# Kernel optimization log

Measured on AMD Instinct MI355X. Metric: run time of the kernel, lower is better.

Reference implementation:

```python
import jax, jax.numpy as jnp
import numpy as np

DIM = 1024
HEADS = 16
HEAD_DIM = DIM // HEADS

def setup_inputs() -> dict:
    key = jax.random.key(0)
    ks = jax.random.split(key, 6)
    s = 0.02
    return {
        "x": jax.random.normal(ks[0], (2, 2048, DIM), dtype=jnp.float32),
        "w_qkv": jax.random.normal(ks[1], (DIM, 3 * DIM), dtype=jnp.float32) * s,
        "w_proj": jax.random.normal(ks[2], (DIM, DIM), dtype=jnp.float32) * s,
        "b_proj": jnp.zeros((DIM,), dtype=jnp.float32),
        "ln_gamma": jnp.ones((DIM,), dtype=jnp.float32),
        "ln_beta": jnp.zeros((DIM,), dtype=jnp.float32),
    }

def layer_norm(x, gamma, beta, eps=1e-5):
    mu = jnp.mean(x, axis=-1, keepdims=True)
    var = jnp.var(x, axis=-1, keepdims=True)
    return (x - mu) * jax.lax.rsqrt(var + eps) * gamma + beta

def reference(x, w_qkv, w_proj, b_proj, ln_gamma, ln_beta):
    B, N, C = x.shape
    residual = x
    h = layer_norm(x, ln_gamma, ln_beta)
    qkv = h @ w_qkv  # [B,N,3C]
    qkv = qkv.reshape(B, N, 3, HEADS, HEAD_DIM)
    q = jnp.transpose(qkv[:, :, 0], (0, 2, 1, 3))  # [B,H,N,D]
    k = jnp.transpose(qkv[:, :, 1], (0, 2, 1, 3))
    v = jnp.transpose(qkv[:, :, 2], (0, 2, 1, 3))
    scale = 1.0 / jnp.sqrt(jnp.float32(HEAD_DIM))
    attn = jnp.einsum('bhqd,bhkd->bhqk', q, k) * scale
    attn = jax.nn.softmax(attn, axis=-1)
    out = jnp.einsum('bhqk,bhkd->bhqd', attn, v)  # [B,H,N,D]
    out = jnp.transpose(out, (0, 2, 1, 3)).reshape(B, N, C)
    out = out @ w_proj + b_proj
    return out + residual
```

## Files before the change

### kernel.cpp

```cpp
#include <hip/hip_runtime.h>

#define DIM   1024
#define HEADS 16
#define HDIM  64
#define BATCH 2
#define SEQ   2048
#define TOK   (BATCH*SEQ)
#define MEG   1048576

typedef __bf16 bf16x8 __attribute__((ext_vector_type(8)));
typedef float  f32x4  __attribute__((ext_vector_type(4)));

__device__ __forceinline__ float b2f(ushort u) {
    union { unsigned int u32; float f; } x; x.u32 = ((unsigned int)u) << 16; return x.f;
}
__device__ __forceinline__ ushort f2b(float f) {
    union { float f; unsigned int u32; } x; x.f = f;
    unsigned int r = x.u32 + 0x7FFFu + ((x.u32 >> 16) & 1u);
    return (ushort)(r >> 16);
}
__device__ __forceinline__ ushort f2b_t(float f) {
    union { float f; unsigned int u32; } x; x.f = f;
    return (ushort)(x.u32 >> 16);
}
__device__ __forceinline__ void gload_lds16(const ushort* g, void* l) {
    __builtin_amdgcn_global_load_lds((const __attribute__((address_space(1))) void*)g,
                                     (__attribute__((address_space(3))) void*)l, 16, 0, 0);
}

__global__ void transpose_f2b_k(const float* __restrict__ src, ushort* __restrict__ dst,
                                int R, int Cc) {
    __shared__ ushort tile[32][33];
    int c0 = blockIdx.x * 32, r0 = blockIdx.y * 32;
    int tx = threadIdx.x, ty = threadIdx.y;
#pragma unroll
    for (int i = 0; i < 4; i++)
        tile[ty + 8 * i][tx] = f2b(src[(long)(r0 + ty + 8 * i) * Cc + c0 + tx]);
    __syncthreads();
#pragma unroll
    for (int i = 0; i < 4; i++)
        dst[(long)(c0 + ty + 8 * i) * R + r0 + tx] = tile[tx][ty + 8 * i];
}

__global__ void transpose_bf16_k(const ushort* __restrict__ src, ushort* __restrict__ dst,
                                 int R, int Cc, long sstride, long dstride) {
    __shared__ ushort tile[32][33];
    long b = blockIdx.z;
    const ushort* s = src + b * sstride;
    ushort* d = dst + b * dstride;
    int c0 = blockIdx.x * 32, r0 = blockIdx.y * 32;
    int tx = threadIdx.x, ty = threadIdx.y;
#pragma unroll
    for (int i = 0; i < 4; i++)
        tile[ty + 8 * i][tx] = s[(long)(r0 + ty + 8 * i) * Cc + c0 + tx];
    __syncthreads();
#pragma unroll
    for (int i = 0; i < 4; i++)
        d[(long)(c0 + ty + 8 * i) * R + r0 + tx] = tile[tx][ty + 8 * i];
}

__global__ __launch_bounds__(256)
void ln_k(const float* __restrict__ x, const float* __restrict__ gamma,
          const float* __restrict__ beta, ushort* __restrict__ h) {
    __shared__ float red[8];
    int row = blockIdx.x, tid = threadIdx.x;
    const float* xr = x + (long)row * DIM;
    float4 xv = *(const float4*)(xr + tid * 4);
    float s1 = xv.x + xv.y + xv.z + xv.w;
    float s2 = xv.x * xv.x + xv.y * xv.y + xv.z * xv.z + xv.w * xv.w;
#pragma unroll
    for (int off = 32; off; off >>= 1) {
        s1 += __shfl_down(s1, off);
        s2 += __shfl_down(s2, off);
    }
    int wid = tid >> 6, lane = tid & 63;
    if (lane == 0) { red[wid * 2] = s1; red[wid * 2 + 1] = s2; }
    __syncthreads();
    s1 = red[0] + red[2] + red[4] + red[6];
    s2 = red[1] + red[3] + red[5] + red[7];
    float mu  = s1 * (1.0f / DIM);
    float var = s2 * (1.0f / DIM) - mu * mu;
    float rs  = rsqrtf(var + 1e-5f);
    float4 gv = *(const float4*)(gamma + tid * 4);
    float4 bv = *(const float4*)(beta + tid * 4);
    ushort4 ov;
    ov.x = f2b((xv.x - mu) * rs * gv.x + bv.x);
    ov.y = f2b((xv.y - mu) * rs * gv.y + bv.y);
    ov.z = f2b((xv.z - mu) * rs * gv.z + bv.z);
    ov.w = f2b((xv.w - mu) * rs * gv.w + bv.w);
    *(ushort4*)(h + (long)row * DIM + tid * 4) = ov;
}

template <int EPI>
__global__ __launch_bounds__(256, 2)
void gemm128_k(const ushort* __restrict__ A, const ushort* __restrict__ Bt,
               int M, int N, int K,
               ushort* __restrict__ qp, ushort* __restrict__ kp, ushort* __restrict__ vp,
               const float* __restrict__ bias, const float* __restrict__ xres,
               float* __restrict__ outp) {
    __shared__ ushort As[128][32];
    __shared__ ushort Bs[128][32];
    int tid  = threadIdx.x;
    int wid  = tid >> 6, lane = tid & 63;
    int quad = lane >> 4, l16 = lane & 15;
    int wm = wid >> 1, wn = wid & 1;
    int rowbase = blockIdx.y * 128;
    int colbase = blockIdx.x * 128;
    int arow = lane >> 2;
    int acol = (lane & 3) * 8;

    f32x4 acc[4][4];
#pragma unroll
    for (int i = 0; i < 4; i++)
#pragma unroll
        for (int j = 0; j < 4; j++) acc[i][j] = (f32x4){0.f, 0.f, 0.f, 0.f};

    for (int k0 = 0; k0 < K; k0 += 32) {
#pragma unroll
        for (int p = 0; p < 2; p++) {
            int c = wid * 2 + p;
            int r = c * 16 + arow;
            const ushort* ga;
            if (EPI == 1) {
                int mm = rowbase + r, cc = k0 + acol;
                int bq = mm >> 11, nn = mm & 2047;
                int head = cc >> 6, d = cc & 63;
                ga = A + ((((long)bq * HEADS + head) * SEQ + nn) << 6) + d;
            } else {
                ga = A + (long)(rowbase + r) * K + k0 + acol;
            }
            gload_lds16(ga, &As[c * 16][0]);
            gload_lds16(Bt + (long)(colbase + r) * K + k0 + acol, &Bs[c * 16][0]);
        }
        __syncthreads();
        bf16x8 fa[4], fb[4];
#pragma unroll
        for (int t = 0; t < 4; t++)
            fa[t] = *(const bf16x8*)(&As[wm * 64 + t * 16 + l16][quad * 8]);
#pragma unroll
        for (int t = 0; t < 4; t++)
            fb[t] = *(const bf16x8*)(&Bs[wn * 64 + t * 16 + l16][quad * 8]);
#pragma unroll
        for (int i = 0; i < 4; i++)
#pragma unroll
            for (int j = 0; j < 4; j++)
                acc[i][j] = __builtin_amdgcn_mfma_f32_16x16x32_bf16(fa[i], fb[j], acc[i][j], 0, 0, 0);
        __syncthreads();
    }

#pragma unroll
    for (int i = 0; i < 4; i++)
#pragma unroll
        for (int j = 0; j < 4; j++) {
            int m0  = rowbase + wm * 64 + i * 16 + quad * 4;
            int col = colbase + wn * 64 + j * 16 + l16;
#pragma unroll
            for (int r = 0; r < 4; r++) {
                float v = acc[i][j][r];
                int mm = m0 + r;
                if (EPI == 0) {
                    int part = col >> 10, rem = col & 1023;
                    int head = rem >> 6, d = rem & 63;
                    int b = mm >> 11, nn = mm & 2047;
                    ushort* dst = (part == 0) ? qp : (part == 1) ? kp : vp;
                    float sv = (part == 0) ? v * 0.125f : v;
                    dst[((((long)b * HEADS + head) * SEQ + nn) << 6) + d] = f2b(sv);
                } else {
                    outp[(long)mm * N + col] = v + bias[col] + xres[(long)mm * N + col];
                }
            }
        }
}

__global__ __launch_bounds__(256, 4)
void attn_k(ushort* qio, const ushort* __restrict__ k,
            const ushort* __restrict__ vt) {
    __shared__ ushort Ks0[2][32][40];
    __shared__ ushort Ks1[2][32][40];
    __shared__ ushort Vs[2][64][40];
    __shared__ ushort plds[4][16][40];
    int bh = blockIdx.y;
    int tid = threadIdx.x, wid = tid >> 6, lane = tid & 63;
    int quad = lane >> 4, l16 = lane & 15;
    ushort* qh = qio + (long)bh * SEQ * HDIM;
    const ushort* kh = k  + (long)bh * SEQ * HDIM;
    const ushort* vh = vt + (long)bh * HDIM * SEQ;

    int krow = tid >> 3, kc8 = (tid & 7) * 8;
    int vrow = tid >> 2, vcol = (tid & 3) * 8;

    int qrow = blockIdx.x * 64 + wid * 16 + l16;
    bf16x8 qf0 = *(const bf16x8*)(qh + (long)qrow * HDIM + quad * 8);
    bf16x8 qf1 = *(const bf16x8*)(qh + (long)qrow * HDIM + 32 + quad * 8);

    f32x4 o[4];
#pragma unroll
    for (int dc = 0; dc < 4; dc++) o[dc] = (f32x4){0.f, 0.f, 0.f, 0.f};
    f32x4 lac0 = (f32x4){0.f, 0.f, 0.f, 0.f};
    f32x4 lac1 = (f32x4){0.f, 0.f, 0.f, 0.f};

    uint4 kreg = *(const uint4*)(kh + (long)krow * HDIM + kc8);
    uint4 vreg = *(const uint4*)(vh + (long)vrow * SEQ + vcol);
    {
        ushort* kdst = (kc8 < 32) ? &Ks0[0][krow][kc8] : &Ks1[0][krow][kc8 - 32];
        *(uint4*)kdst = kreg;
        *(uint4*)(&Vs[0][vrow][vcol]) = vreg;
    }

    const int NIT = SEQ / 32;
    for (int it = 0; it < NIT; ++it) {
        int buf = it & 1;
        if (it + 1 < NIT) {
            int kt = (it + 1) * 32;
            kreg = *(const uint4*)(kh + (long)(kt + krow) * HDIM + kc8);
            vreg = *(const uint4*)(vh + (long)vrow * SEQ + kt + vcol);
        }
        __syncthreads();

        bf16x8 kb00 = *(const bf16x8*)(&Ks0[buf][l16][quad * 8]);
        bf16x8 kb01 = *(const bf16x8*)(&Ks1[buf][l16][quad * 8]);
        bf16x8 kb10 = *(const bf16x8*)(&Ks0[buf][16 + l16][quad * 8]);
        bf16x8 kb11 = *(const bf16x8*)(&Ks1[buf][16 + l16][quad * 8]);
        f32x4 s0 = (f32x4){0.f, 0.f, 0.f, 0.f};
        f32x4 s1 = (f32x4){0.f, 0.f, 0.f, 0.f};
        s0 = __builtin_amdgcn_mfma_f32_16x16x32_bf16(qf0, kb00, s0, 0, 0, 0);
        s0 = __builtin_amdgcn_mfma_f32_16x16x32_bf16(qf1, kb01, s0, 0, 0, 0);
        s1 = __builtin_amdgcn_mfma_f32_16x16x32_bf16(qf0, kb10, s1, 0, 0, 0);
        s1 = __builtin_amdgcn_mfma_f32_16x16x32_bf16(qf1, kb11, s1, 0, 0, 0);

        float p0[4], p1[4];
#pragma unroll
        for (int r = 0; r < 4; r++) {
            p0[r] = __expf(s0[r]);
            p1[r] = __expf(s1[r]);
            lac0[r] += p0[r];
            lac1[r] += p1[r];
        }
#pragma unroll
        for (int r = 0; r < 4; r++) {
            plds[wid][quad * 4 + r][l16]      = f2b_t(p0[r]);
            plds[wid][quad * 4 + r][16 + l16] = f2b_t(p1[r]);
        }
        asm volatile("s_waitcnt lgkmcnt(0)" ::: "memory");
        bf16x8 pf = *(const bf16x8*)(&plds[wid][l16][quad * 8]);
#pragma unroll
        for (int dc = 0; dc < 4; dc++) {
            bf16x8 vfb = *(const bf16x8*)(&Vs[buf][dc * 16 + l16][quad * 8]);
            o[dc] = __builtin_amdgcn_mfma_f32_16x16x32_bf16(pf, vfb, o[dc], 0, 0, 0);
        }

        if (it + 1 < NIT) {
            ushort* kdst = (kc8 < 32) ? &Ks0[buf ^ 1][krow][kc8] : &Ks1[buf ^ 1][krow][kc8 - 32];
            *(uint4*)kdst = kreg;
            *(uint4*)(&Vs[buf ^ 1][vrow][vcol]) = vreg;
        }
    }

    float linv[4];
#pragma unroll
    for (int r = 0; r < 4; r++) {
        float t = lac0[r] + lac1[r];
        t += __shfl_xor(t, 1);
        t += __shfl_xor(t, 2);
        t += __shfl_xor(t, 4);
        t += __shfl_xor(t, 8);
        linv[r] = 1.0f / t;
    }

    int rowo = blockIdx.x * 64 + wid * 16 + quad * 4;
#pragma unroll
    for (int dc = 0; dc < 4; dc++)
#pragma unroll
        for (int r = 0; r < 4; r++)
            qh[(long)(rowo + r) * HDIM + dc * 16 + l16] = f2b(o[dc][r] * linv[r]);
}

extern "C" void kernel_launch(void* const* d_in, const int* in_sizes, int n_in,
                              void* d_out, int out_size, void* d_ws, size_t ws_size,
                              hipStream_t stream) {
    const float* x      = (const float*)d_in[0];
    const float* w_qkv  = (const float*)d_in[1];
    const float* w_proj = (const float*)d_in[2];
    const float* b_proj = (const float*)d_in[3];
    const float* gamma  = (const float*)d_in[4];
    const float* beta   = (const float*)d_in[5];
    float* out = (float*)d_out;

    ushort* ws   = (ushort*)d_ws;
    ushort* h_vt = ws;
    ushort* wqt  = ws + (size_t)4 * MEG;
    ushort* qb   = ws + (size_t)7 * MEG;
    ushort* kb   = ws + (size_t)11 * MEG;
    ushort* vb   = ws + (size_t)15 * MEG;

    transpose_f2b_k<<<dim3(3 * DIM / 32, DIM / 32), dim3(32, 8), 0, stream>>>(
        w_qkv, wqt, DIM, 3 * DIM);
    ln_k<<<dim3(TOK), dim3(256), 0, stream>>>(x, gamma, beta, h_vt);
    gemm128_k<0><<<dim3(3 * DIM / 128, TOK / 128), dim3(256), 0, stream>>>(
        h_vt, wqt, TOK, 3 * DIM, DIM, qb, kb, vb, nullptr, nullptr, nullptr);
    transpose_bf16_k<<<dim3(HDIM / 32, SEQ / 32, BATCH * HEADS), dim3(32, 8), 0, stream>>>(
        vb, h_vt, SEQ, HDIM, (long)SEQ * HDIM, (long)SEQ * HDIM);
    attn_k<<<dim3(SEQ / 64, BATCH * HEADS), dim3(256), 0, stream>>>(qb, kb, h_vt);
    transpose_f2b_k<<<dim3(DIM / 32, DIM / 32), dim3(32, 8), 0, stream>>>(
        w_proj, kb, DIM, DIM);
    gemm128_k<1><<<dim3(DIM / 128, TOK / 128), dim3(256), 0, stream>>>(
        qb, kb, TOK, DIM, DIM, nullptr, nullptr, nullptr, b_proj, x, out);
}
```

Baseline: 224.6 us.

## Process two query sub-tiles per wave in attention to reuse K/V tiles

Each wave in the attention kernel now handles 32 query rows (two 16-row sub-tiles) instead of 16, so every K and V fragment read from LDS feeds twice as many MFMAs. Blocks cover 128 queries and the grid is halved, which cuts global K/V traffic per query. The K tile is repacked into a flat padded panel array, and launch bounds are relaxed to allow more registers. The cost is fewer blocks (512) and higher register pressure, which can lower occupancy and latency hiding.

```diff
diff --git a/kernel.cpp b/kernel.cpp
--- a/kernel.cpp
+++ b/kernel.cpp
@@ -172,13 +172,12 @@
         }
 }
 
-__global__ __launch_bounds__(256, 4)
+__global__ __launch_bounds__(256, 1)
 void attn_k(ushort* qio, const ushort* __restrict__ k,
             const ushort* __restrict__ vt) {
-    __shared__ ushort Ks0[2][32][40];
-    __shared__ ushort Ks1[2][32][40];
+    __shared__ ushort Kp[2][2][1312];
     __shared__ ushort Vs[2][64][40];
-    __shared__ ushort plds[4][16][40];
+    __shared__ ushort plds[4][2][16][40];
     int bh = blockIdx.y;
     int tid = threadIdx.x, wid = tid >> 6, lane = tid & 63;
     int quad = lane >> 4, l16 = lane & 15;
@@ -187,25 +186,32 @@
     const ushort* vh = vt + (long)bh * HDIM * SEQ;
 
     int krow = tid >> 3, kc8 = (tid & 7) * 8;
+    int kpan = kc8 >> 5, kcp = kc8 & 31;
+    int koff = krow * 40 + kcp;
     int vrow = tid >> 2, vcol = (tid & 3) * 8;
 
-    int qrow = blockIdx.x * 64 + wid * 16 + l16;
-    bf16x8 qf0 = *(const bf16x8*)(qh + (long)qrow * HDIM + quad * 8);
-    bf16x8 qf1 = *(const bf16x8*)(qh + (long)qrow * HDIM + 32 + quad * 8);
-
-    f32x4 o[4];
-#pragma unroll
-    for (int dc = 0; dc < 4; dc++) o[dc] = (f32x4){0.f, 0.f, 0.f, 0.f};
-    f32x4 lac0 = (f32x4){0.f, 0.f, 0.f, 0.f};
-    f32x4 lac1 = (f32x4){0.f, 0.f, 0.f, 0.f};
+    int qrow0 = blockIdx.x * 128 + wid * 32;
+    bf16x8 qf[2][2];
+#pragma unroll
+    for (int s = 0; s < 2; s++) {
+        qf[s][0] = *(const bf16x8*)(qh + (long)(qrow0 + s * 16 + l16) * HDIM + quad * 8);
+        qf[s][1] = *(const bf16x8*)(qh + (long)(qrow0 + s * 16 + l16) * HDIM + 32 + quad * 8);
+    }
+
+    f32x4 o[2][4];
+    f32x4 lac[2][2];
+#pragma unroll
+    for (int s = 0; s < 2; s++) {
+#pragma unroll
+        for (int dc = 0; dc < 4; dc++) o[s][dc] = (f32x4){0.f, 0.f, 0.f, 0.f};
+        lac[s][0] = (f32x4){0.f, 0.f, 0.f, 0.f};
+        lac[s][1] = (f32x4){0.f, 0.f, 0.f, 0.f};
+    }
 
     uint4 kreg = *(const uint4*)(kh + (long)krow * HDIM + kc8);
     uint4 vreg = *(const uint4*)(vh + (long)vrow * SEQ + vcol);
-    {
-        ushort* kdst = (kc8 < 32) ? &Ks0[0][krow][kc8] : &Ks1[0][krow][kc8 - 32];
-        *(uint4*)kdst = kreg;
-        *(uint4*)(&Vs[0][vrow][vcol]) = vreg;
-    }
+    *(uint4*)(&Kp[0][kpan][koff]) = kreg;
+    *(uint4*)(&Vs[0][vrow][vcol]) = vreg;
 
     const int NIT = SEQ / 32;
     for (int it = 0; it < NIT; ++it) {
@@ -217,62 +223,74 @@
         }
         __syncthreads();
 
-        bf16x8 kb00 = *(const bf16x8*)(&Ks0[buf][l16][quad * 8]);
-        bf16x8 kb01 = *(const bf16x8*)(&Ks1[buf][l16][quad * 8]);
-        bf16x8 kb10 = *(const bf16x8*)(&Ks0[buf][16 + l16][quad * 8]);
-        bf16x8 kb11 = *(const bf16x8*)(&Ks1[buf][16 + l16][quad * 8]);
-        f32x4 s0 = (f32x4){0.f, 0.f, 0.f, 0.f};
-        f32x4 s1 = (f32x4){0.f, 0.f, 0.f, 0.f};
-        s0 = __builtin_amdgcn_mfma_f32_16x16x32_bf16(qf0, kb00, s0, 0, 0, 0);
-        s0 = __builtin_amdgcn_mfma_f32_16x16x32_bf16(qf1, kb01, s0, 0, 0, 0);
-        s1 = __builtin_amdgcn_mfma_f32_16x16x32_bf16(qf0, kb10, s1, 0, 0, 0);
-        s1 = __builtin_amdgcn_mfma_f32_16x16x32_bf16(qf1, kb11, s1, 0, 0, 0);
-
-        float p0[4], p1[4];
-#pragma unroll
-        for (int r = 0; r < 4; r++) {
-            p0[r] = __expf(s0[r]);
-            p1[r] = __expf(s1[r]);
-            lac0[r] += p0[r];
-            lac1[r] += p1[r];
-        }
-#pragma unroll
-        for (int r = 0; r < 4; r++) {
-            plds[wid][quad * 4 + r][l16]      = f2b_t(p0[r]);
-            plds[wid][quad * 4 + r][16 + l16] = f2b_t(p1[r]);
-        }
+        bf16x8 kb[2][2];
+#pragma unroll
+        for (int t = 0; t < 2; t++)
+#pragma unroll
+            for (int p = 0; p < 2; p++)
+                kb[t][p] = *(const bf16x8*)(&Kp[buf][p][(t * 16 + l16) * 40 + quad * 8]);
+
+        f32x4 sc[2][2];
+#pragma unroll
+        for (int s = 0; s < 2; s++)
+#pragma unroll
+            for (int t = 0; t < 2; t++) {
+                f32x4 z = (f32x4){0.f, 0.f, 0.f, 0.f};
+                z = __builtin_amdgcn_mfma_f32_16x16x32_bf16(qf[s][0], kb[t][0], z, 0, 0, 0);
+                z = __builtin_amdgcn_mfma_f32_16x16x32_bf16(qf[s][1], kb[t][1], z, 0, 0, 0);
+                sc[s][t] = z;
+            }
+
+#pragma unroll
+        for (int s = 0; s < 2; s++)
+#pragma unroll
+            for (int r = 0; r < 4; r++) {
+                float p0 = __expf(sc[s][0][r]);
+                float p1 = __expf(sc[s][1][r]);
+                lac[s][0][r] += p0;
+                lac[s][1][r] += p1;
+                plds[wid][s][quad * 4 + r][l16]      = f2b_t(p0);
+                plds[wid][s][quad * 4 + r][16 + l16] = f2b_t(p1);
+            }
         asm volatile("s_waitcnt lgkmcnt(0)" ::: "memory");
-        bf16x8 pf = *(const bf16x8*)(&plds[wid][l16][quad * 8]);
+
+        bf16x8 pf[2];
+#pragma unroll
+        for (int s = 0; s < 2; s++)
+            pf[s] = *(const bf16x8*)(&plds[wid][s][l16][quad * 8]);
 #pragma unroll
         for (int dc = 0; dc < 4; dc++) {
             bf16x8 vfb = *(const bf16x8*)(&Vs[buf][dc * 16 + l16][quad * 8]);
-            o[dc] = __builtin_amdgcn_mfma_f32_16x16x32_bf16(pf, vfb, o[dc], 0, 0, 0);
+#pragma unroll
+            for (int s = 0; s < 2; s++)
+                o[s][dc] = __builtin_amdgcn_mfma_f32_16x16x32_bf16(pf[s], vfb, o[s][dc], 0, 0, 0);
         }
 
         if (it + 1 < NIT) {
-            ushort* kdst = (kc8 < 32) ? &Ks0[buf ^ 1][krow][kc8] : &Ks1[buf ^ 1][krow][kc8 - 32];
-            *(uint4*)kdst = kreg;
+            *(uint4*)(&Kp[buf ^ 1][kpan][koff]) = kreg;
             *(uint4*)(&Vs[buf ^ 1][vrow][vcol]) = vreg;
         }
     }
 
-    float linv[4];
-#pragma unroll
-    for (int r = 0; r < 4; r++) {
-        float t = lac0[r] + lac1[r];
-        t += __shfl_xor(t, 1);
-        t += __shfl_xor(t, 2);
-        t += __shfl_xor(t, 4);
-        t += __shfl_xor(t, 8);
-        linv[r] = 1.0f / t;
-    }
-
-    int rowo = blockIdx.x * 64 + wid * 16 + quad * 4;
-#pragma unroll
-    for (int dc = 0; dc < 4; dc++)
-#pragma unroll
-        for (int r = 0; r < 4; r++)
-            qh[(long)(rowo + r) * HDIM + dc * 16 + l16] = f2b(o[dc][r] * linv[r]);
+#pragma unroll
+    for (int s = 0; s < 2; s++) {
+        float linv[4];
+#pragma unroll
+        for (int r = 0; r < 4; r++) {
+            float t = lac[s][0][r] + lac[s][1][r];
+            t += __shfl_xor(t, 1);
+            t += __shfl_xor(t, 2);
+            t += __shfl_xor(t, 4);
+            t += __shfl_xor(t, 8);
+            linv[r] = 1.0f / t;
+        }
+        int rowo = qrow0 + s * 16 + quad * 4;
+#pragma unroll
+        for (int dc = 0; dc < 4; dc++)
+#pragma unroll
+            for (int r = 0; r < 4; r++)
+                qh[(long)(rowo + r) * HDIM + dc * 16 + l16] = f2b(o[s][dc][r] * linv[r]);
+    }
 }
 
 extern "C" void kernel_launch(void* const* d_in, const int* in_sizes, int n_in,
@@ -300,7 +318,7 @@
         h_vt, wqt, TOK, 3 * DIM, DIM, qb, kb, vb, nullptr, nullptr, nullptr);
     transpose_bf16_k<<<dim3(HDIM / 32, SEQ / 32, BATCH * HEADS), dim3(32, 8), 0, stream>>>(
         vb, h_vt, SEQ, HDIM, (long)SEQ * HDIM, (long)SEQ * HDIM);
-    attn_k<<<dim3(SEQ / 64, BATCH * HEADS), dim3(256), 0, stream>>>(qb, kb, h_vt);
+    attn_k<<<dim3(SEQ / 128, BATCH * HEADS), dim3(256), 0, stream>>>(qb, kb, h_vt);
     transpose_f2b_k<<<dim3(DIM / 32, DIM / 32), dim3(32, 8), 0, stream>>>(
         w_proj, kb, DIM, DIM);
     gemm128_k<1><<<dim3(DIM / 128, TOK / 128), dim3(256), 0, stream>>>(
```

Measured after the change: 225.7 us. No clear change (+0.5%).
